# Kernel tuning notes

Measured on AMD Instinct MI355X. Metric: run time of the kernel, lower is better.

The kernel has to match this reference:

```python
import jax, jax.numpy as jnp
import numpy as np

B, S, A, C, M, CE = 2, 8, 24000, 80, 20, 7
POS_TH, NEG_TH = 0.5, 0.4
V0, V1 = 0.1, 0.2              # SSD encode variances
SL1_BETA = 1.0 / 9.0
ALPHA, GAMMA = 0.25, 2.0
CB_BETA = 0.9999
EPS = 1e-7


def point_form(cf):
    # (cx,cy,w,h) -> (x1,y1,x2,y2)
    return jnp.concatenate([cf[..., :2] - cf[..., 2:] * 0.5, cf[..., :2] + cf[..., 2:] * 0.5], -1)


def jaccard(a, b):
    # a: [M,4], b: [A,4] point form -> IoU [M,A]
    lt = jnp.maximum(a[:, None, :2], b[None, :, :2])
    rb = jnp.minimum(a[:, None, 2:], b[None, :, 2:])
    wh = jnp.clip(rb - lt, 0.0)
    inter = wh[..., 0] * wh[..., 1]
    aa = (a[:, 2] - a[:, 0]) * (a[:, 3] - a[:, 1])
    ab = (b[:, 2] - b[:, 0]) * (b[:, 3] - b[:, 1])
    return inter / (aa[:, None] + ab[None, :] - inter + 1e-10)


def encode(matched, anchors_cf):
    # matched: [A,4] point form gt, anchors_cf: [A,4] center form
    g_cxcy = ((matched[:, :2] + matched[:, 2:]) * 0.5 - anchors_cf[:, :2]) / (V0 * anchors_cf[:, 2:])
    g_wh = jnp.log(jnp.clip(matched[:, 2:] - matched[:, :2], 1e-6) / anchors_cf[:, 2:]) / V1
    return jnp.concatenate([g_cxcy, g_wh], -1)


def bce(p, y):
    p = jnp.clip(p, EPS, 1.0 - EPS)
    return -(y * jnp.log(p) + (1.0 - y) * jnp.log1p(-p))


def match_one(gtb, gtl, count, anchors_pf, anchors_cf):
    # SSD-style match with ignore band: conf in {-1 ignore, 0 background, i+1 positive matched to gt i}
    valid = jnp.arange(M) < count
    iou = jnp.where(valid[:, None], jaccard(gtb, anchors_pf), -1.0)  # [M,A]
    best_prior_idx = jnp.argmax(iou, axis=1)                         # best anchor per gt
    best_truth_iou = jnp.max(iou, axis=0)                            # best gt per anchor
    best_truth_idx = jnp.argmax(iou, axis=0)
    sidx = jnp.where(valid, best_prior_idx, A)                       # out-of-range -> dropped
    best_truth_iou = best_truth_iou.at[sidx].set(2.0, mode='drop')   # force each gt's best anchor positive
    best_truth_idx = best_truth_idx.at[sidx].set(jnp.arange(M), mode='drop')
    conf = (best_truth_idx + 1).astype(jnp.int32)                    # dummy labels = gt index
    conf = jnp.where(best_truth_iou < POS_TH, -1, conf)
    conf = jnp.where(best_truth_iou < NEG_TH, 0, conf)
    loc = encode(gtb[best_truth_idx], anchors_cf)
    has = count > 0
    conf = jnp.where(has, conf, -1)                                  # empty frame -> all ignore
    loc = jnp.where(has, loc, 0.0)
    # gather per-anchor multi-hot labels: labels_bs = [zeros; gt_labels][dumy_conf]
    lab = jnp.where((conf > 0)[:, None], gtl[jnp.clip(conf - 1, 0, M - 1)], 0.0)
    return conf, loc, lab


def setup_inputs() -> dict:
    key = jax.random.key(0)
    ks = jax.random.split(key, 10)
    confidence = jax.random.normal(ks[0], (B, S, A, C), jnp.float32)
    predicted_locations = jax.random.normal(ks[1], (B, S, A, 4), jnp.float32)
    gc = jax.random.uniform(ks[2], (B, S, M, 2))
    gw = jax.random.uniform(ks[3], (B, S, M, 2), minval=0.05, maxval=0.4)
    gt_boxes = jnp.clip(jnp.concatenate([gc - gw * 0.5, gc + gw * 0.5], -1), 0.0, 1.0)
    gt_labels = (jax.random.uniform(ks[4], (B, S, M, C)) < 0.05).astype(jnp.float32)
    counts = jax.random.randint(ks[5], (B, S), 0, M + 1, jnp.int32)
    ac = jax.random.uniform(ks[6], (A, 2))
    aw = jax.random.uniform(ks[7], (A, 2), minval=0.02, maxval=0.3)
    anchors = jnp.concatenate([ac, aw], -1)  # center form (cx,cy,w,h)
    ego_preds = jax.random.normal(ks[8], (B, S, CE), jnp.float32)
    ego_labels = jax.random.randint(ks[9], (B, S), 0, CE, jnp.int32)
    cls_num_list = jax.random.randint(jax.random.fold_in(key, 11), (C,), 1, 10000, jnp.int32)
    return {"confidence": confidence, "predicted_locations": predicted_locations,
            "gt_boxes": gt_boxes, "gt_labels": gt_labels, "counts": counts,
            "anchors": anchors, "ego_preds": ego_preds, "ego_labels": ego_labels,
            "cls_num_list": cls_num_list}


def reference(confidence, predicted_locations, gt_boxes, gt_labels, counts, anchors, ego_preds, ego_labels, cls_num_list):
    preds = jax.nn.sigmoid(confidence)
    anchors_pf = point_form(anchors)
    flat = lambda x: x.reshape((B * S,) + x.shape[2:])
    conf_t, loc_t, lab_t = jax.vmap(match_one, in_axes=(0, 0, 0, None, None))(
        flat(gt_boxes), flat(gt_labels), counts.reshape(-1), anchors_pf, anchors)
    labels_bin = jax.lax.stop_gradient(conf_t.reshape(B, S, A).astype(jnp.float32))
    gt_locations = jax.lax.stop_gradient(loc_t.reshape(B, S, A, 4))
    all_labels = jax.lax.stop_gradient(lab_t.reshape(B, S, A, C))

    pos = (labels_bin > 0).astype(jnp.float32)
    num_pos = jnp.maximum(1.0, pos.sum())
    n = jnp.abs(predicted_locations - gt_locations)
    sl1 = jnp.where(n < SL1_BETA, 0.5 * n * n / SL1_BETA, n - 0.5 * SL1_BETA)
    regression_loss = (sl1 * pos[..., None]).sum() / (num_pos * 4.0)

    # class-balanced focal loss (module hardcodes gamma=1 inside sigmoid_cb_focal_loss)
    cmask = (labels_bin > -1).astype(jnp.float32)[..., None]
    w = (1.0 - CB_BETA) / (1.0 - jnp.power(jnp.float32(CB_BETA), cls_num_list.astype(jnp.float32)))
    w = w / w.sum()
    y = all_labels
    pt = preds * y + (1.0 - preds) * (1.0 - y)
    cb = w * y + (1.0 - CB_BETA) * (1.0 - y)
    cls_loss = (bce(preds, y) * cb * (1.0 - pt) * cmask).sum() / num_pos

    # ego focal loss (replicates original get_one_hot_labels column semantics)
    ep = jax.nn.sigmoid(ego_preds)
    evalid = ego_labels > -1
    col = (jnp.where(evalid[..., None], jax.nn.one_hot(ego_labels, CE), 0.0).sum((0, 1)) > 0).astype(jnp.float32)
    oh = jnp.broadcast_to(col, ep.shape)
    af = ALPHA * oh + (1.0 - ALPHA) * (1.0 - oh)
    ept = ep * oh + (1.0 - ep) * (1.0 - oh)
    n_ego = evalid.sum().astype(jnp.float32)
    ego_sum = (bce(ep, oh) * af * (1.0 - ept) ** GAMMA * evalid[..., None].astype(jnp.float32)).sum()
    ego_loss = jnp.where(n_ego > 0, ego_sum / jnp.maximum(n_ego, 1.0), 0.0)

    return regression_loss, cls_loss / 8.0 + ego_loss / 4.0
```

## Files before the change

kernel.cpp:

```cpp
#include <hip/hip_runtime.h>
#include <math.h>

#define NB 2
#define NS 8
#define NA 24000
#define NC 80
#define NM 20
#define NCE 7
#define NBS (NB*NS)
#define CPB 75
#define APC (NA/CPB)
#define F4PC (APC*NC/4)

#define POS_TH 0.5f
#define NEG_TH 0.4f
#define OMB 1e-4f

__device__ inline unsigned long long packKey(float f, unsigned idx) {
    unsigned u = __float_as_uint(f);
    u = (u & 0x80000000u) ? ~u : (u | 0x80000000u);
    return ((unsigned long long)u << 32) | (unsigned long long)(0xFFFFFFFFu - idx);
}

__global__ void __launch_bounds__(256)
k_iou(const float* __restrict__ gtb, const int* __restrict__ counts,
      const float* __restrict__ anchors,
      float* __restrict__ bt_iou, int* __restrict__ bt_idx,
      unsigned long long* __restrict__ chunkbest,
      double* __restrict__ acc, int* __restrict__ npos) {
    int bid = blockIdx.x;
    int bs = bid / CPB;
    int chunk = bid % CPB;
    int t = threadIdx.x;
    int cnt = counts[bs];

    if (bid == 0 && t == 0) { acc[0] = 0.0; acc[1] = 0.0; *npos = 0; }

    __shared__ float sg[NM][5];
    if (t < NM) {
        const float* g = gtb + ((size_t)bs * NM + t) * 4;
        float x1 = g[0], y1 = g[1], x2 = g[2], y2 = g[3];
        sg[t][0] = x1; sg[t][1] = y1; sg[t][2] = x2; sg[t][3] = y2;
        sg[t][4] = (x2 - x1) * (y2 - y1);
    }
    __syncthreads();

    unsigned long long bp[NM];
    #pragma unroll
    for (int m = 0; m < NM; m++) bp[m] = 0ULL;

    int a0 = chunk * APC;
    for (int a = a0 + t; a < a0 + APC; a += 256) {
        float4 cf = ((const float4*)anchors)[a];
        float ax1 = cf.x - cf.z * 0.5f, ay1 = cf.y - cf.w * 0.5f;
        float ax2 = cf.x + cf.z * 0.5f, ay2 = cf.y + cf.w * 0.5f;
        float aarea = (ax2 - ax1) * (ay2 - ay1);
        float best = -1.0f; int bm = 0;
        #pragma unroll
        for (int m = 0; m < NM; m++) {
            if (m < cnt) {
                float ltx = fmaxf(sg[m][0], ax1), lty = fmaxf(sg[m][1], ay1);
                float rbx = fminf(sg[m][2], ax2), rby = fminf(sg[m][3], ay2);
                float wx = fmaxf(rbx - ltx, 0.0f), wy = fmaxf(rby - lty, 0.0f);
                float inter = wx * wy;
                float iou = inter / (sg[m][4] + aarea - inter + 1e-10f);
                if (iou > best) { best = iou; bm = m; }
                unsigned long long k = packKey(iou, (unsigned)a);
                if (k > bp[m]) bp[m] = k;
            }
        }
        bt_iou[(size_t)bs * NA + a] = best;
        bt_idx[(size_t)bs * NA + a] = bm;
    }

    __shared__ unsigned long long sk[4][NM];
    int wave = t >> 6, lane = t & 63;
    for (int m = 0; m < cnt; m++) {
        unsigned long long k = bp[m];
        #pragma unroll
        for (int off = 32; off > 0; off >>= 1) {
            unsigned long long o = __shfl_xor(k, off);
            if (o > k) k = o;
        }
        if (lane == 0) sk[wave][m] = k;
    }
    __syncthreads();
    if (t < NM) {
        unsigned long long k = 0ULL;
        if (t < cnt) {
            k = sk[0][t];
            if (sk[1][t] > k) k = sk[1][t];
            if (sk[2][t] > k) k = sk[2][t];
            if (sk[3][t] > k) k = sk[3][t];
        }
        chunkbest[bid * NM + t] = k;
    }
}

__global__ void __launch_bounds__(256)
k_match(const float* __restrict__ gtb, const int* __restrict__ counts,
        const float* __restrict__ anchors, const float* __restrict__ ploc,
        const float* __restrict__ gtl, const float* __restrict__ logits,
        const int* __restrict__ cls_num,
        const unsigned long long* __restrict__ chunkbest,
        const float* __restrict__ bt_iou, const int* __restrict__ bt_idx,
        double* __restrict__ acc, int* __restrict__ npos) {
    int bid = blockIdx.x;
    int bs = bid / CPB;
    int chunk = bid % CPB;
    int t = threadIdx.x;
    int cnt = counts[bs];

    __shared__ float sg[NM][4];
    __shared__ unsigned abest[NM];
    __shared__ float wsh[NC];
    __shared__ float wsum_sh;
    __shared__ float smask[APC];
    if (t < NM) {
        const float* g = gtb + ((size_t)bs * NM + t) * 4;
        sg[t][0] = g[0]; sg[t][1] = g[1]; sg[t][2] = g[2]; sg[t][3] = g[3];
    }
    if (t < NC) {
        float n = (float)cls_num[t];
        wsh[t] = OMB / (1.0f - powf(0.9999f, n));
    }
    if (t < NM && t < cnt) {
        unsigned long long k = 0ULL;
        for (int c = 0; c < CPB; c++) {
            unsigned long long o = chunkbest[(bs * CPB + c) * NM + t];
            if (o > k) k = o;
        }
        abest[t] = 0xFFFFFFFFu - (unsigned)(k & 0xFFFFFFFFull);
    }
    __syncthreads();
    if (t == 0) {
        float s = 0.0f;
        for (int c = 0; c < NC; c++) s += wsh[c];
        wsum_sh = s;
    }
    __syncthreads();
    if (t < NC) wsh[t] = wsh[t] / wsum_sh;

    const float SL1B = 1.0f / 9.0f;
    float regsum = 0.0f, corrsum = 0.0f;
    int pcnt = 0;
    int a0 = chunk * APC;
    for (int al = t; al < APC; al += 256) {
        int a = a0 + al;
        size_t ia = (size_t)bs * NA + a;
        float iou = bt_iou[ia];
        int idx = bt_idx[ia];
        for (int m = 0; m < cnt; m++) {
            if (abest[m] == (unsigned)a) { iou = 2.0f; idx = m; }
        }
        int code;
        if (cnt == 0) code = -1;
        else if (iou < NEG_TH) code = 0;
        else if (iou < POS_TH) code = -1;
        else code = idx + 1;
        smask[al] = (code == -1) ? 0.0f : 1.0f;
        if (code > 0) {
            pcnt++;
            float4 cf = ((const float4*)anchors)[a];
            float mx1 = sg[idx][0], my1 = sg[idx][1], mx2 = sg[idx][2], my2 = sg[idx][3];
            float g0 = ((mx1 + mx2) * 0.5f - cf.x) / (0.1f * cf.z);
            float g1 = ((my1 + my2) * 0.5f - cf.y) / (0.1f * cf.w);
            float g2 = logf(fmaxf(mx2 - mx1, 1e-6f) / cf.z) / 0.2f;
            float g3 = logf(fmaxf(my2 - my1, 1e-6f) / cf.w) / 0.2f;
            float4 p = ((const float4*)ploc)[ia];
            float n0 = fabsf(p.x - g0), n1 = fabsf(p.y - g1);
            float n2 = fabsf(p.z - g2), n3 = fabsf(p.w - g3);
            float s0 = n0 < SL1B ? 0.5f * n0 * n0 / SL1B : n0 - 0.5f * SL1B;
            float s1 = n1 < SL1B ? 0.5f * n1 * n1 / SL1B : n1 - 0.5f * SL1B;
            float s2 = n2 < SL1B ? 0.5f * n2 * n2 / SL1B : n2 - 0.5f * SL1B;
            float s3 = n3 < SL1B ? 0.5f * n3 * n3 / SL1B : n3 - 0.5f * SL1B;
            regsum += s0 + s1 + s2 + s3;

            const float4* yrow = (const float4*)(gtl + ((size_t)(bs * NM + idx)) * NC);
            const float4* xrow = (const float4*)(logits + ia * NC);
            #pragma unroll 4
            for (int c4 = 0; c4 < NC / 4; c4++) {
                float4 y4 = yrow[c4];
                if (y4.x > 0.5f || y4.y > 0.5f || y4.z > 0.5f || y4.w > 0.5f) {
                    float4 x4 = xrow[c4];
                    float yv[4] = {y4.x, y4.y, y4.z, y4.w};
                    float xv[4] = {x4.x, x4.y, x4.z, x4.w};
                    #pragma unroll
                    for (int j = 0; j < 4; j++) {
                        if (yv[j] > 0.5f) {
                            float x = xv[j];
                            float e = __expf(-x);
                            float s = 1.0f + e;
                            float pr = __builtin_amdgcn_rcpf(s);
                            float ls = __logf(s);
                            corrsum += ls * wsh[c4 * 4 + j] * (e * pr)
                                     - OMB * (x + ls) * pr;
                        }
                    }
                }
            }
        }
    }
    __syncthreads();

    const float4* x4p = (const float4*)logits + ((size_t)bs * NA + a0) * (NC / 4);
    float bgsum = 0.0f;
    #pragma unroll
    for (int g = 0; g < 5; g++) {
        float4 xs[5];
        float  ms[5];
        #pragma unroll
        for (int j = 0; j < 5; j++) {
            int i = t + (g * 5 + j) * 256;
            ms[j] = smask[i / 20];
            xs[j] = x4p[i];
        }
        #pragma unroll
        for (int j = 0; j < 5; j++) {
            float xv[4] = {xs[j].x, xs[j].y, xs[j].z, xs[j].w};
            float tsum = 0.0f;
            #pragma unroll
            for (int jj = 0; jj < 4; jj++) {
                float x = xv[jj];
                float e = __expf(-x);
                float s = 1.0f + e;
                float pr = __builtin_amdgcn_rcpf(s);
                float ls = __logf(s);
                tsum += (x + ls) * pr;
            }
            bgsum = fmaf(ms[j], tsum, bgsum);
        }
    }
    float clssum = corrsum + OMB * bgsum;

    #pragma unroll
    for (int off = 32; off > 0; off >>= 1) {
        regsum += __shfl_xor(regsum, off);
        clssum += __shfl_xor(clssum, off);
        pcnt   += __shfl_xor(pcnt, off);
    }
    __shared__ float sf[4], sc[4];
    __shared__ int   si[4];
    int wave = t >> 6, lane = t & 63;
    if (lane == 0) { sf[wave] = regsum; sc[wave] = clssum; si[wave] = pcnt; }
    __syncthreads();
    if (t == 0) {
        atomicAdd(&acc[0], (double)(sf[0] + sf[1] + sf[2] + sf[3]));
        atomicAdd(&acc[1], (double)(sc[0] + sc[1] + sc[2] + sc[3]));
        atomicAdd(npos, si[0] + si[1] + si[2] + si[3]);
    }
}

__global__ void k_final(const float* __restrict__ ego_preds, const int* __restrict__ ego_labels,
                        const double* __restrict__ acc, const int* __restrict__ npos,
                        float* __restrict__ out) {
    __shared__ float scol[NCE];
    __shared__ float sred[128];
    __shared__ int   sval[128];
    const float EPSF = 1e-7f;
    int t = threadIdx.x;
    if (t < NCE) {
        float c = 0.0f;
        for (int i = 0; i < NBS; i++) {
            int l = ego_labels[i];
            if (l > -1 && l == t) c = 1.0f;
        }
        scol[t] = c;
    }
    __syncthreads();

    float term = 0.0f;
    if (t < NBS * NCE) {
        int bs = t / NCE, e = t % NCE;
        int lbl = ego_labels[bs];
        if (lbl > -1) {
            float x = ego_preds[t];
            float ep = 1.0f / (1.0f + expf(-x));
            float oh = scol[e];
            float af = 0.25f * oh + 0.75f * (1.0f - oh);
            float ept = ep * oh + (1.0f - ep) * (1.0f - oh);
            float epc = fminf(fmaxf(ep, EPSF), 1.0f - EPSF);
            float bce = -(oh * logf(epc) + (1.0f - oh) * log1pf(-epc));
            float om = 1.0f - ept;
            term = bce * af * om * om;
        }
    }
    sred[t] = term;
    sval[t] = (t < NBS && ego_labels[t] > -1) ? 1 : 0;
    __syncthreads();
    for (int off = 64; off > 0; off >>= 1) {
        if (t < off) { sred[t] += sred[t + off]; sval[t] += sval[t + off]; }
        __syncthreads();
    }
    if (t == 0) {
        float esum = sred[0];
        int ne = sval[0];
        float ego = (ne > 0) ? esum / (float)(ne > 1 ? ne : 1) : 0.0f;
        double npd = (double)(*npos);
        if (npd < 1.0) npd = 1.0;
        out[0] = (float)(acc[0] / (npd * 4.0));
        out[1] = (float)(acc[1] / npd / 8.0 + (double)ego / 4.0);
    }
}

extern "C" void kernel_launch(void* const* d_in, const int* in_sizes, int n_in,
                              void* d_out, int out_size, void* d_ws, size_t ws_size,
                              hipStream_t stream) {
    const float* confidence = (const float*)d_in[0];
    const float* ploc       = (const float*)d_in[1];
    const float* gtb        = (const float*)d_in[2];
    const float* gtl        = (const float*)d_in[3];
    const int*   counts     = (const int*)d_in[4];
    const float* anchors    = (const float*)d_in[5];
    const float* ego_preds  = (const float*)d_in[6];
    const int*   ego_labels = (const int*)d_in[7];
    const int*   cls_num    = (const int*)d_in[8];
    float* out = (float*)d_out;

    char* ws = (char*)d_ws;
    double* acc  = (double*)ws;
    int* npos    = (int*)(ws + 16);
    unsigned long long* chunkbest = (unsigned long long*)(ws + 64);
    float* bt_iou = (float*)(ws + 64 + 192000);
    int*   bt_idx = (int*)(ws + 64 + 192000 + 1536000);

    k_iou<<<NBS * CPB, 256, 0, stream>>>(gtb, counts, anchors, bt_iou, bt_idx,
                                         chunkbest, acc, npos);
    k_match<<<NBS * CPB, 256, 0, stream>>>(gtb, counts, anchors, ploc, gtl, confidence,
                                           cls_num, chunkbest, bt_iou, bt_idx, acc, npos);
    k_final<<<1, 128, 0, stream>>>(ego_preds, ego_labels, acc, npos, out);
}
```

Baseline: 271.9 us.

## Split background class pass into its own grid and hoist per-sample prep

A single-block prep kernel now computes, once, the class-balanced weights and the per-ground-truth best-anchor reduction over chunks. Before, every match block redid both. The match kernel writes a per-anchor mask into the IoU buffer instead of shared memory. A new grid-stride kernel with 2000 blocks then streams all logits to compute the masked background focal term. The goal is to remove redundant serial reductions and to spread the bandwidth-heavy logits read over more blocks. The cost is two extra kernel launches and a global round trip for the mask.

```diff
diff --git a/kernel.cpp b/kernel.cpp
--- a/kernel.cpp
+++ b/kernel.cpp
@@ -10,11 +10,14 @@
 #define NBS (NB*NS)
 #define CPB 75
 #define APC (NA/CPB)
-#define F4PC (APC*NC/4)
 
 #define POS_TH 0.5f
 #define NEG_TH 0.4f
 #define OMB 1e-4f
+
+#define CLS_BLOCKS 2000
+#define CLS_GSZ (CLS_BLOCKS*256)
+#define CLS_PT 15
 
 __device__ inline unsigned long long packKey(float f, unsigned idx) {
     unsigned u = __float_as_uint(f);
@@ -26,15 +29,12 @@
 k_iou(const float* __restrict__ gtb, const int* __restrict__ counts,
       const float* __restrict__ anchors,
       float* __restrict__ bt_iou, int* __restrict__ bt_idx,
-      unsigned long long* __restrict__ chunkbest,
-      double* __restrict__ acc, int* __restrict__ npos) {
+      unsigned long long* __restrict__ chunkbest) {
     int bid = blockIdx.x;
     int bs = bid / CPB;
     int chunk = bid % CPB;
     int t = threadIdx.x;
     int cnt = counts[bs];
-
-    if (bid == 0 && t == 0) { acc[0] = 0.0; acc[1] = 0.0; *npos = 0; }
 
     __shared__ float sg[NM][5];
     if (t < NM) {
@@ -97,13 +97,43 @@
     }
 }
 
+__global__ void k_prep(const int* __restrict__ cls_num,
+                       const unsigned long long* __restrict__ chunkbest,
+                       float* __restrict__ wsn, unsigned* __restrict__ gbest,
+                       double* __restrict__ acc, int* __restrict__ npos) {
+    __shared__ float wsh[NC];
+    __shared__ float wsum_sh;
+    int t = threadIdx.x;
+    if (t == 0) { acc[0] = 0.0; acc[1] = 0.0; *npos = 0; }
+    if (t < NC) {
+        float n = (float)cls_num[t];
+        wsh[t] = OMB / (1.0f - powf(0.9999f, n));
+    }
+    if (t < NBS * NM) {
+        int bs = t / NM, m = t % NM;
+        unsigned long long k = 0ULL;
+        for (int c = 0; c < CPB; c++) {
+            unsigned long long o = chunkbest[(bs * CPB + c) * NM + m];
+            if (o > k) k = o;
+        }
+        gbest[t] = 0xFFFFFFFFu - (unsigned)(k & 0xFFFFFFFFull);
+    }
+    __syncthreads();
+    if (t == 0) {
+        float s = 0.0f;
+        for (int c = 0; c < NC; c++) s += wsh[c];
+        wsum_sh = s;
+    }
+    __syncthreads();
+    if (t < NC) wsn[t] = wsh[t] / wsum_sh;
+}
+
 __global__ void __launch_bounds__(256)
 k_match(const float* __restrict__ gtb, const int* __restrict__ counts,
         const float* __restrict__ anchors, const float* __restrict__ ploc,
         const float* __restrict__ gtl, const float* __restrict__ logits,
-        const int* __restrict__ cls_num,
-        const unsigned long long* __restrict__ chunkbest,
-        const float* __restrict__ bt_iou, const int* __restrict__ bt_idx,
+        const float* __restrict__ wsn, const unsigned* __restrict__ gbest,
+        float* bt_iou , const int* __restrict__ bt_idx,
         double* __restrict__ acc, int* __restrict__ npos) {
     int bid = blockIdx.x;
     int bs = bid / CPB;
@@ -113,33 +143,12 @@
 
     __shared__ float sg[NM][4];
     __shared__ unsigned abest[NM];
-    __shared__ float wsh[NC];
-    __shared__ float wsum_sh;
-    __shared__ float smask[APC];
     if (t < NM) {
         const float* g = gtb + ((size_t)bs * NM + t) * 4;
         sg[t][0] = g[0]; sg[t][1] = g[1]; sg[t][2] = g[2]; sg[t][3] = g[3];
-    }
-    if (t < NC) {
-        float n = (float)cls_num[t];
-        wsh[t] = OMB / (1.0f - powf(0.9999f, n));
-    }
-    if (t < NM && t < cnt) {
-        unsigned long long k = 0ULL;
-        for (int c = 0; c < CPB; c++) {
-            unsigned long long o = chunkbest[(bs * CPB + c) * NM + t];
-            if (o > k) k = o;
-        }
-        abest[t] = 0xFFFFFFFFu - (unsigned)(k & 0xFFFFFFFFull);
-    }
-    __syncthreads();
-    if (t == 0) {
-        float s = 0.0f;
-        for (int c = 0; c < NC; c++) s += wsh[c];
-        wsum_sh = s;
-    }
-    __syncthreads();
-    if (t < NC) wsh[t] = wsh[t] / wsum_sh;
+        abest[t] = gbest[bs * NM + t];
+    }
+    __syncthreads();
 
     const float SL1B = 1.0f / 9.0f;
     float regsum = 0.0f, corrsum = 0.0f;
@@ -158,7 +167,7 @@
         else if (iou < NEG_TH) code = 0;
         else if (iou < POS_TH) code = -1;
         else code = idx + 1;
-        smask[al] = (code == -1) ? 0.0f : 1.0f;
+        bt_iou[ia] = (code == -1) ? 0.0f : 1.0f;
         if (code > 0) {
             pcnt++;
             float4 cf = ((const float4*)anchors)[a];
@@ -193,7 +202,7 @@
                             float s = 1.0f + e;
                             float pr = __builtin_amdgcn_rcpf(s);
                             float ls = __logf(s);
-                            corrsum += ls * wsh[c4 * 4 + j] * (e * pr)
+                            corrsum += ls * wsn[c4 * 4 + j] * (e * pr)
                                      - OMB * (x + ls) * pr;
                         }
                     }
@@ -201,18 +210,39 @@
             }
         }
     }
-    __syncthreads();
-
-    const float4* x4p = (const float4*)logits + ((size_t)bs * NA + a0) * (NC / 4);
+
+    #pragma unroll
+    for (int off = 32; off > 0; off >>= 1) {
+        regsum  += __shfl_xor(regsum, off);
+        corrsum += __shfl_xor(corrsum, off);
+        pcnt    += __shfl_xor(pcnt, off);
+    }
+    __shared__ float sf[4], sc[4];
+    __shared__ int   si[4];
+    int wave = t >> 6, lane = t & 63;
+    if (lane == 0) { sf[wave] = regsum; sc[wave] = corrsum; si[wave] = pcnt; }
+    __syncthreads();
+    if (t == 0) {
+        atomicAdd(&acc[0], (double)(sf[0] + sf[1] + sf[2] + sf[3]));
+        atomicAdd(&acc[1], (double)(sc[0] + sc[1] + sc[2] + sc[3]));
+        atomicAdd(npos, si[0] + si[1] + si[2] + si[3]);
+    }
+}
+
+__global__ void __launch_bounds__(256, 8)
+k_cls(const float* __restrict__ logits, const float* __restrict__ cmask,
+      double* __restrict__ acc) {
+    int gid = blockIdx.x * 256 + threadIdx.x;
+    const float4* x4p = (const float4*)logits;
     float bgsum = 0.0f;
     #pragma unroll
-    for (int g = 0; g < 5; g++) {
+    for (int g = 0; g < 3; g++) {
         float4 xs[5];
         float  ms[5];
         #pragma unroll
         for (int j = 0; j < 5; j++) {
-            int i = t + (g * 5 + j) * 256;
-            ms[j] = smask[i / 20];
+            int i = gid + (g * 5 + j) * CLS_GSZ;
+            ms[j] = cmask[i / 20];
             xs[j] = x4p[i];
         }
         #pragma unroll
@@ -231,24 +261,14 @@
             bgsum = fmaf(ms[j], tsum, bgsum);
         }
     }
-    float clssum = corrsum + OMB * bgsum;
 
     #pragma unroll
-    for (int off = 32; off > 0; off >>= 1) {
-        regsum += __shfl_xor(regsum, off);
-        clssum += __shfl_xor(clssum, off);
-        pcnt   += __shfl_xor(pcnt, off);
-    }
-    __shared__ float sf[4], sc[4];
-    __shared__ int   si[4];
-    int wave = t >> 6, lane = t & 63;
-    if (lane == 0) { sf[wave] = regsum; sc[wave] = clssum; si[wave] = pcnt; }
-    __syncthreads();
-    if (t == 0) {
-        atomicAdd(&acc[0], (double)(sf[0] + sf[1] + sf[2] + sf[3]));
-        atomicAdd(&acc[1], (double)(sc[0] + sc[1] + sc[2] + sc[3]));
-        atomicAdd(npos, si[0] + si[1] + si[2] + si[3]);
-    }
+    for (int off = 32; off > 0; off >>= 1) bgsum += __shfl_xor(bgsum, off);
+    __shared__ float sb[4];
+    int t = threadIdx.x, wave = t >> 6, lane = t & 63;
+    if (lane == 0) sb[wave] = bgsum;
+    __syncthreads();
+    if (t == 0) atomicAdd(&acc[1], (double)(OMB * (sb[0] + sb[1] + sb[2] + sb[3])));
 }
 
 __global__ void k_final(const float* __restrict__ ego_preds, const int* __restrict__ ego_labels,
@@ -323,10 +343,13 @@
     unsigned long long* chunkbest = (unsigned long long*)(ws + 64);
     float* bt_iou = (float*)(ws + 64 + 192000);
     int*   bt_idx = (int*)(ws + 64 + 192000 + 1536000);
-
-    k_iou<<<NBS * CPB, 256, 0, stream>>>(gtb, counts, anchors, bt_iou, bt_idx,
-                                         chunkbest, acc, npos);
+    float* wsn    = (float*)(ws + 64 + 192000 + 1536000 + 1536000);
+    unsigned* gbest = (unsigned*)(ws + 64 + 192000 + 1536000 + 1536000 + 320);
+
+    k_iou<<<NBS * CPB, 256, 0, stream>>>(gtb, counts, anchors, bt_iou, bt_idx, chunkbest);
+    k_prep<<<1, 384, 0, stream>>>(cls_num, chunkbest, wsn, gbest, acc, npos);
     k_match<<<NBS * CPB, 256, 0, stream>>>(gtb, counts, anchors, ploc, gtl, confidence,
-                                           cls_num, chunkbest, bt_iou, bt_idx, acc, npos);
+                                           wsn, gbest, bt_iou, bt_idx, acc, npos);
+    k_cls<<<CLS_BLOCKS, 256, 0, stream>>>(confidence, bt_iou, acc);
     k_final<<<1, 128, 0, stream>>>(ego_preds, ego_labels, acc, npos, out);
 }
```

Result: slower. 305.6 us (+12.4%).

## Move unmasked background logit sum into IoU kernel and subtract ignored rows later

Applied to the files above, without the earlier changes.

The full-logit background sum moves into the first (IoU) kernel and is computed without the ignore mask, so it no longer depends on matching. The match kernel then subtracts the contribution of ignored anchors row by row. A new single-block prep kernel reduces the per-chunk partial sums, the best-anchor keys and the class weights once, instead of every match block redoing that work. This overlaps the large logit read with the IoU phase, at the cost of an extra launch and a double-precision reduction.

```diff
diff --git a/kernel.cpp b/kernel.cpp
--- a/kernel.cpp
+++ b/kernel.cpp
@@ -23,18 +23,16 @@
 }
 
 __global__ void __launch_bounds__(256)
-k_iou(const float* __restrict__ gtb, const int* __restrict__ counts,
-      const float* __restrict__ anchors,
-      float* __restrict__ bt_iou, int* __restrict__ bt_idx,
-      unsigned long long* __restrict__ chunkbest,
-      double* __restrict__ acc, int* __restrict__ npos) {
+k_main(const float* __restrict__ gtb, const int* __restrict__ counts,
+       const float* __restrict__ anchors, const float* __restrict__ logits,
+       float* __restrict__ bt_iou, int* __restrict__ bt_idx,
+       unsigned long long* __restrict__ chunkbest,
+       double* __restrict__ bgpart) {
     int bid = blockIdx.x;
     int bs = bid / CPB;
     int chunk = bid % CPB;
     int t = threadIdx.x;
     int cnt = counts[bs];
-
-    if (bid == 0 && t == 0) { acc[0] = 0.0; acc[1] = 0.0; *npos = 0; }
 
     __shared__ float sg[NM][5];
     if (t < NM) {
@@ -95,14 +93,85 @@
         }
         chunkbest[bid * NM + t] = k;
     }
+
+    const float4* x4p = (const float4*)logits + ((size_t)bs * NA + a0) * (NC / 4);
+    double bg = 0.0;
+    #pragma unroll
+    for (int g = 0; g < 5; g++) {
+        float4 xs[5];
+        #pragma unroll
+        for (int j = 0; j < 5; j++) xs[j] = x4p[t + (g * 5 + j) * 256];
+        #pragma unroll
+        for (int j = 0; j < 5; j++) {
+            float xv[4] = {xs[j].x, xs[j].y, xs[j].z, xs[j].w};
+            float tsum = 0.0f;
+            #pragma unroll
+            for (int jj = 0; jj < 4; jj++) {
+                float x = xv[jj];
+                float e = __expf(-x);
+                float s = 1.0f + e;
+                float pr = __builtin_amdgcn_rcpf(s);
+                float ls = __logf(s);
+                tsum += (x + ls) * pr;
+            }
+            bg += (double)tsum;
+        }
+    }
+    #pragma unroll
+    for (int off = 32; off > 0; off >>= 1) bg += __shfl_xor(bg, off);
+    __shared__ double sb[4];
+    if (lane == 0) sb[wave] = bg;
+    __syncthreads();
+    if (t == 0) bgpart[bid] = sb[0] + sb[1] + sb[2] + sb[3];
+}
+
+__global__ void k_prep(const int* __restrict__ cls_num,
+                       const unsigned long long* __restrict__ chunkbest,
+                       const double* __restrict__ bgpart,
+                       float* __restrict__ wsn, unsigned* __restrict__ gbest,
+                       double* __restrict__ acc, int* __restrict__ npos) {
+    __shared__ float wsh[NC];
+    __shared__ float wsum_sh;
+    __shared__ double sred[6];
+    int t = threadIdx.x;
+    if (t == 0) { acc[0] = 0.0; *npos = 0; }
+    if (t < NC) {
+        float n = (float)cls_num[t];
+        wsh[t] = OMB / (1.0f - powf(0.9999f, n));
+    }
+    if (t < NBS * NM) {
+        int bs = t / NM, m = t % NM;
+        unsigned long long k = 0ULL;
+        for (int c = 0; c < CPB; c++) {
+            unsigned long long o = chunkbest[(bs * CPB + c) * NM + m];
+            if (o > k) k = o;
+        }
+        gbest[t] = 0xFFFFFFFFu - (unsigned)(k & 0xFFFFFFFFull);
+    }
+    double b = 0.0;
+    for (int i = t; i < NBS * CPB; i += 384) b += bgpart[i];
+    #pragma unroll
+    for (int off = 32; off > 0; off >>= 1) b += __shfl_xor(b, off);
+    int wave = t >> 6, lane = t & 63;
+    if (lane == 0) sred[wave] = b;
+    __syncthreads();
+    if (t == 0) {
+        double s = 0.0;
+        for (int w = 0; w < 6; w++) s += sred[w];
+        acc[1] = (double)OMB * s;
+        float ws = 0.0f;
+        for (int c = 0; c < NC; c++) ws += wsh[c];
+        wsum_sh = ws;
+    }
+    __syncthreads();
+    if (t < NC) wsn[t] = wsh[t] / wsum_sh;
 }
 
 __global__ void __launch_bounds__(256)
 k_match(const float* __restrict__ gtb, const int* __restrict__ counts,
         const float* __restrict__ anchors, const float* __restrict__ ploc,
         const float* __restrict__ gtl, const float* __restrict__ logits,
-        const int* __restrict__ cls_num,
-        const unsigned long long* __restrict__ chunkbest,
+        const float* __restrict__ wsn, const unsigned* __restrict__ gbest,
         const float* __restrict__ bt_iou, const int* __restrict__ bt_idx,
         double* __restrict__ acc, int* __restrict__ npos) {
     int bid = blockIdx.x;
@@ -113,36 +182,15 @@
 
     __shared__ float sg[NM][4];
     __shared__ unsigned abest[NM];
-    __shared__ float wsh[NC];
-    __shared__ float wsum_sh;
-    __shared__ float smask[APC];
     if (t < NM) {
         const float* g = gtb + ((size_t)bs * NM + t) * 4;
         sg[t][0] = g[0]; sg[t][1] = g[1]; sg[t][2] = g[2]; sg[t][3] = g[3];
-    }
-    if (t < NC) {
-        float n = (float)cls_num[t];
-        wsh[t] = OMB / (1.0f - powf(0.9999f, n));
-    }
-    if (t < NM && t < cnt) {
-        unsigned long long k = 0ULL;
-        for (int c = 0; c < CPB; c++) {
-            unsigned long long o = chunkbest[(bs * CPB + c) * NM + t];
-            if (o > k) k = o;
-        }
-        abest[t] = 0xFFFFFFFFu - (unsigned)(k & 0xFFFFFFFFull);
-    }
-    __syncthreads();
-    if (t == 0) {
-        float s = 0.0f;
-        for (int c = 0; c < NC; c++) s += wsh[c];
-        wsum_sh = s;
-    }
-    __syncthreads();
-    if (t < NC) wsh[t] = wsh[t] / wsum_sh;
+        abest[t] = gbest[bs * NM + t];
+    }
+    __syncthreads();
 
     const float SL1B = 1.0f / 9.0f;
-    float regsum = 0.0f, corrsum = 0.0f;
+    float regsum = 0.0f, corrsum = 0.0f, negsum = 0.0f;
     int pcnt = 0;
     int a0 = chunk * APC;
     for (int al = t; al < APC; al += 256) {
@@ -158,7 +206,6 @@
         else if (iou < NEG_TH) code = 0;
         else if (iou < POS_TH) code = -1;
         else code = idx + 1;
-        smask[al] = (code == -1) ? 0.0f : 1.0f;
         if (code > 0) {
             pcnt++;
             float4 cf = ((const float4*)anchors)[a];
@@ -193,46 +240,34 @@
                             float s = 1.0f + e;
                             float pr = __builtin_amdgcn_rcpf(s);
                             float ls = __logf(s);
-                            corrsum += ls * wsh[c4 * 4 + j] * (e * pr)
+                            corrsum += ls * wsn[c4 * 4 + j] * (e * pr)
                                      - OMB * (x + ls) * pr;
                         }
                     }
                 }
             }
-        }
-    }
-    __syncthreads();
-
-    const float4* x4p = (const float4*)logits + ((size_t)bs * NA + a0) * (NC / 4);
-    float bgsum = 0.0f;
-    #pragma unroll
-    for (int g = 0; g < 5; g++) {
-        float4 xs[5];
-        float  ms[5];
-        #pragma unroll
-        for (int j = 0; j < 5; j++) {
-            int i = t + (g * 5 + j) * 256;
-            ms[j] = smask[i / 20];
-            xs[j] = x4p[i];
-        }
-        #pragma unroll
-        for (int j = 0; j < 5; j++) {
-            float xv[4] = {xs[j].x, xs[j].y, xs[j].z, xs[j].w};
-            float tsum = 0.0f;
-            #pragma unroll
-            for (int jj = 0; jj < 4; jj++) {
-                float x = xv[jj];
-                float e = __expf(-x);
-                float s = 1.0f + e;
-                float pr = __builtin_amdgcn_rcpf(s);
-                float ls = __logf(s);
-                tsum += (x + ls) * pr;
+        } else if (code == -1) {
+            const float4* xrow = (const float4*)(logits + ia * NC);
+            float rs = 0.0f;
+            #pragma unroll 5
+            for (int c4 = 0; c4 < NC / 4; c4++) {
+                float4 x4 = xrow[c4];
+                float xv[4] = {x4.x, x4.y, x4.z, x4.w};
+                #pragma unroll
+                for (int j = 0; j < 4; j++) {
+                    float x = xv[j];
+                    float e = __expf(-x);
+                    float s = 1.0f + e;
+                    float pr = __builtin_amdgcn_rcpf(s);
+                    float ls = __logf(s);
+                    rs += (x + ls) * pr;
+                }
             }
-            bgsum = fmaf(ms[j], tsum, bgsum);
-        }
-    }
-    float clssum = corrsum + OMB * bgsum;
-
+            negsum += rs;
+        }
+    }
+
+    float clssum = corrsum - OMB * negsum;
     #pragma unroll
     for (int off = 32; off > 0; off >>= 1) {
         regsum += __shfl_xor(regsum, off);
@@ -323,10 +358,14 @@
     unsigned long long* chunkbest = (unsigned long long*)(ws + 64);
     float* bt_iou = (float*)(ws + 64 + 192000);
     int*   bt_idx = (int*)(ws + 64 + 192000 + 1536000);
-
-    k_iou<<<NBS * CPB, 256, 0, stream>>>(gtb, counts, anchors, bt_iou, bt_idx,
-                                         chunkbest, acc, npos);
+    float* wsn    = (float*)(ws + 64 + 192000 + 1536000 + 1536000);
+    unsigned* gbest = (unsigned*)(ws + 64 + 192000 + 1536000 + 1536000 + 320);
+    double* bgpart  = (double*)(ws + 64 + 192000 + 1536000 + 1536000 + 320 + 1280);
+
+    k_main<<<NBS * CPB, 256, 0, stream>>>(gtb, counts, anchors, confidence,
+                                          bt_iou, bt_idx, chunkbest, bgpart);
+    k_prep<<<1, 384, 0, stream>>>(cls_num, chunkbest, bgpart, wsn, gbest, acc, npos);
     k_match<<<NBS * CPB, 256, 0, stream>>>(gtb, counts, anchors, ploc, gtl, confidence,
-                                           cls_num, chunkbest, bt_iou, bt_idx, acc, npos);
+                                           wsn, gbest, bt_iou, bt_idx, acc, npos);
     k_final<<<1, 128, 0, stream>>>(ego_preds, ego_labels, acc, npos, out);
 }
```

Result: slower. 305.3 us (+12.3%).

## Recompute IoU in match kernel, atomicMax per-gt best, defer positive class work

Applied to the files above, without the earlier changes.

The first kernel no longer writes per-anchor best IoU and index to global memory. It only computes each gt's best anchor and merges it with a global atomicMax, and the match kernel recomputes the per-anchor IoU argmax itself. Positive anchors are queued in shared memory, and their class correction terms are processed cooperatively after the background pass, which removes divergent per-thread 80-class loops. Logit loads use nontemporal hints, a memset replaces the in-kernel accumulator init, and launch bounds request 5 blocks per CU. The cost is duplicated IoU arithmetic, plus a shared-memory atomic and queue in the match kernel.

```diff
diff --git a/kernel.cpp b/kernel.cpp
--- a/kernel.cpp
+++ b/kernel.cpp
@@ -10,7 +10,6 @@
 #define NBS (NB*NS)
 #define CPB 75
 #define APC (NA/CPB)
-#define F4PC (APC*NC/4)
 
 #define POS_TH 0.5f
 #define NEG_TH 0.4f
@@ -22,19 +21,21 @@
     return ((unsigned long long)u << 32) | (unsigned long long)(0xFFFFFFFFu - idx);
 }
 
+typedef float v4f __attribute__((ext_vector_type(4)));
+__device__ inline float4 ntload4(const float4* p) {
+    v4f v = __builtin_nontemporal_load((const v4f*)p);
+    return make_float4(v.x, v.y, v.z, v.w);
+}
+
 __global__ void __launch_bounds__(256)
-k_iou(const float* __restrict__ gtb, const int* __restrict__ counts,
-      const float* __restrict__ anchors,
-      float* __restrict__ bt_iou, int* __restrict__ bt_idx,
-      unsigned long long* __restrict__ chunkbest,
-      double* __restrict__ acc, int* __restrict__ npos) {
+k_gbest(const float* __restrict__ gtb, const int* __restrict__ counts,
+        const float* __restrict__ anchors, unsigned long long* __restrict__ gbest) {
     int bid = blockIdx.x;
     int bs = bid / CPB;
     int chunk = bid % CPB;
     int t = threadIdx.x;
     int cnt = counts[bs];
-
-    if (bid == 0 && t == 0) { acc[0] = 0.0; acc[1] = 0.0; *npos = 0; }
+    if (cnt == 0) return;
 
     __shared__ float sg[NM][5];
     if (t < NM) {
@@ -45,38 +46,39 @@
     }
     __syncthreads();
 
-    unsigned long long bp[NM];
-    #pragma unroll
-    for (int m = 0; m < NM; m++) bp[m] = 0ULL;
-
     int a0 = chunk * APC;
-    for (int a = a0 + t; a < a0 + APC; a += 256) {
-        float4 cf = ((const float4*)anchors)[a];
-        float ax1 = cf.x - cf.z * 0.5f, ay1 = cf.y - cf.w * 0.5f;
-        float ax2 = cf.x + cf.z * 0.5f, ay2 = cf.y + cf.w * 0.5f;
-        float aarea = (ax2 - ax1) * (ay2 - ay1);
-        float best = -1.0f; int bm = 0;
-        #pragma unroll
-        for (int m = 0; m < NM; m++) {
-            if (m < cnt) {
-                float ltx = fmaxf(sg[m][0], ax1), lty = fmaxf(sg[m][1], ay1);
-                float rbx = fminf(sg[m][2], ax2), rby = fminf(sg[m][3], ay2);
-                float wx = fmaxf(rbx - ltx, 0.0f), wy = fmaxf(rby - lty, 0.0f);
-                float inter = wx * wy;
-                float iou = inter / (sg[m][4] + aarea - inter + 1e-10f);
-                if (iou > best) { best = iou; bm = m; }
-                unsigned long long k = packKey(iou, (unsigned)a);
-                if (k > bp[m]) bp[m] = k;
-            }
-        }
-        bt_iou[(size_t)bs * NA + a] = best;
-        bt_idx[(size_t)bs * NA + a] = bm;
+    bool has2 = t < (APC - 256);
+    float4 c1 = ((const float4*)anchors)[a0 + t];
+    float bx1 = c1.x - c1.z * 0.5f, by1 = c1.y - c1.w * 0.5f;
+    float bx2 = c1.x + c1.z * 0.5f, by2 = c1.y + c1.w * 0.5f;
+    float bar = (bx2 - bx1) * (by2 - by1);
+    float cx1 = 0, cy1 = 0, cx2 = 0, cy2 = 0, car = 0;
+    if (has2) {
+        float4 c2 = ((const float4*)anchors)[a0 + 256 + t];
+        cx1 = c2.x - c2.z * 0.5f; cy1 = c2.y - c2.w * 0.5f;
+        cx2 = c2.x + c2.z * 0.5f; cy2 = c2.y + c2.w * 0.5f;
+        car = (cx2 - cx1) * (cy2 - cy1);
     }
 
     __shared__ unsigned long long sk[4][NM];
     int wave = t >> 6, lane = t & 63;
     for (int m = 0; m < cnt; m++) {
-        unsigned long long k = bp[m];
+        float gx1 = sg[m][0], gy1 = sg[m][1], gx2 = sg[m][2], gy2 = sg[m][3], gar = sg[m][4];
+        float ltx = fmaxf(gx1, bx1), lty = fmaxf(gy1, by1);
+        float rbx = fminf(gx2, bx2), rby = fminf(gy2, by2);
+        float wx = fmaxf(rbx - ltx, 0.0f), wy = fmaxf(rby - lty, 0.0f);
+        float inter = wx * wy;
+        float iou = inter / (gar + bar - inter + 1e-10f);
+        unsigned long long k = packKey(iou, (unsigned)(a0 + t));
+        if (has2) {
+            float ltx2 = fmaxf(gx1, cx1), lty2 = fmaxf(gy1, cy1);
+            float rbx2 = fminf(gx2, cx2), rby2 = fminf(gy2, cy2);
+            float wx2 = fmaxf(rbx2 - ltx2, 0.0f), wy2 = fmaxf(rby2 - lty2, 0.0f);
+            float inter2 = wx2 * wy2;
+            float iou2 = inter2 / (gar + car - inter2 + 1e-10f);
+            unsigned long long k2 = packKey(iou2, (unsigned)(a0 + 256 + t));
+            if (k2 > k) k = k2;
+        }
         #pragma unroll
         for (int off = 32; off > 0; off >>= 1) {
             unsigned long long o = __shfl_xor(k, off);
@@ -85,25 +87,21 @@
         if (lane == 0) sk[wave][m] = k;
     }
     __syncthreads();
-    if (t < NM) {
-        unsigned long long k = 0ULL;
-        if (t < cnt) {
-            k = sk[0][t];
-            if (sk[1][t] > k) k = sk[1][t];
-            if (sk[2][t] > k) k = sk[2][t];
-            if (sk[3][t] > k) k = sk[3][t];
-        }
-        chunkbest[bid * NM + t] = k;
-    }
-}
-
-__global__ void __launch_bounds__(256)
+    if (t < cnt) {
+        unsigned long long k = sk[0][t];
+        if (sk[1][t] > k) k = sk[1][t];
+        if (sk[2][t] > k) k = sk[2][t];
+        if (sk[3][t] > k) k = sk[3][t];
+        atomicMax(&gbest[bs * NM + t], k);
+    }
+}
+
+__global__ void __launch_bounds__(256, 5)
 k_match(const float* __restrict__ gtb, const int* __restrict__ counts,
         const float* __restrict__ anchors, const float* __restrict__ ploc,
         const float* __restrict__ gtl, const float* __restrict__ logits,
         const int* __restrict__ cls_num,
-        const unsigned long long* __restrict__ chunkbest,
-        const float* __restrict__ bt_iou, const int* __restrict__ bt_idx,
+        const unsigned long long* __restrict__ gbest,
         double* __restrict__ acc, int* __restrict__ npos) {
     int bid = blockIdx.x;
     int bs = bid / CPB;
@@ -111,26 +109,25 @@
     int t = threadIdx.x;
     int cnt = counts[bs];
 
-    __shared__ float sg[NM][4];
+    __shared__ float sg[NM][5];
     __shared__ unsigned abest[NM];
     __shared__ float wsh[NC];
     __shared__ float wsum_sh;
     __shared__ float smask[APC];
+    __shared__ unsigned qpos[APC];
+    __shared__ int npq;
+    if (t == 0) npq = 0;
     if (t < NM) {
         const float* g = gtb + ((size_t)bs * NM + t) * 4;
-        sg[t][0] = g[0]; sg[t][1] = g[1]; sg[t][2] = g[2]; sg[t][3] = g[3];
+        float x1 = g[0], y1 = g[1], x2 = g[2], y2 = g[3];
+        sg[t][0] = x1; sg[t][1] = y1; sg[t][2] = x2; sg[t][3] = y2;
+        sg[t][4] = (x2 - x1) * (y2 - y1);
+        if (t < cnt)
+            abest[t] = 0xFFFFFFFFu - (unsigned)(gbest[bs * NM + t] & 0xFFFFFFFFull);
     }
     if (t < NC) {
         float n = (float)cls_num[t];
         wsh[t] = OMB / (1.0f - powf(0.9999f, n));
-    }
-    if (t < NM && t < cnt) {
-        unsigned long long k = 0ULL;
-        for (int c = 0; c < CPB; c++) {
-            unsigned long long o = chunkbest[(bs * CPB + c) * NM + t];
-            if (o > k) k = o;
-        }
-        abest[t] = 0xFFFFFFFFu - (unsigned)(k & 0xFFFFFFFFull);
     }
     __syncthreads();
     if (t == 0) {
@@ -142,27 +139,37 @@
     if (t < NC) wsh[t] = wsh[t] / wsum_sh;
 
     const float SL1B = 1.0f / 9.0f;
-    float regsum = 0.0f, corrsum = 0.0f;
+    float regsum = 0.0f;
     int pcnt = 0;
     int a0 = chunk * APC;
     for (int al = t; al < APC; al += 256) {
         int a = a0 + al;
-        size_t ia = (size_t)bs * NA + a;
-        float iou = bt_iou[ia];
-        int idx = bt_idx[ia];
+        float4 cf = ((const float4*)anchors)[a];
+        float ax1 = cf.x - cf.z * 0.5f, ay1 = cf.y - cf.w * 0.5f;
+        float ax2 = cf.x + cf.z * 0.5f, ay2 = cf.y + cf.w * 0.5f;
+        float aarea = (ax2 - ax1) * (ay2 - ay1);
+        float best = -1.0f; int bm = 0;
         for (int m = 0; m < cnt; m++) {
-            if (abest[m] == (unsigned)a) { iou = 2.0f; idx = m; }
+            float ltx = fmaxf(sg[m][0], ax1), lty = fmaxf(sg[m][1], ay1);
+            float rbx = fminf(sg[m][2], ax2), rby = fminf(sg[m][3], ay2);
+            float wx = fmaxf(rbx - ltx, 0.0f), wy = fmaxf(rby - lty, 0.0f);
+            float inter = wx * wy;
+            float iou = inter / (sg[m][4] + aarea - inter + 1e-10f);
+            if (iou > best) { best = iou; bm = m; }
+        }
+        for (int m = 0; m < cnt; m++) {
+            if (abest[m] == (unsigned)a) { best = 2.0f; bm = m; }
         }
         int code;
         if (cnt == 0) code = -1;
-        else if (iou < NEG_TH) code = 0;
-        else if (iou < POS_TH) code = -1;
-        else code = idx + 1;
+        else if (best < NEG_TH) code = 0;
+        else if (best < POS_TH) code = -1;
+        else code = bm + 1;
         smask[al] = (code == -1) ? 0.0f : 1.0f;
         if (code > 0) {
             pcnt++;
-            float4 cf = ((const float4*)anchors)[a];
-            float mx1 = sg[idx][0], my1 = sg[idx][1], mx2 = sg[idx][2], my2 = sg[idx][3];
+            size_t ia = (size_t)bs * NA + a;
+            float mx1 = sg[bm][0], my1 = sg[bm][1], mx2 = sg[bm][2], my2 = sg[bm][3];
             float g0 = ((mx1 + mx2) * 0.5f - cf.x) / (0.1f * cf.z);
             float g1 = ((my1 + my2) * 0.5f - cf.y) / (0.1f * cf.w);
             float g2 = logf(fmaxf(mx2 - mx1, 1e-6f) / cf.z) / 0.2f;
@@ -175,30 +182,8 @@
             float s2 = n2 < SL1B ? 0.5f * n2 * n2 / SL1B : n2 - 0.5f * SL1B;
             float s3 = n3 < SL1B ? 0.5f * n3 * n3 / SL1B : n3 - 0.5f * SL1B;
             regsum += s0 + s1 + s2 + s3;
-
-            const float4* yrow = (const float4*)(gtl + ((size_t)(bs * NM + idx)) * NC);
-            const float4* xrow = (const float4*)(logits + ia * NC);
-            #pragma unroll 4
-            for (int c4 = 0; c4 < NC / 4; c4++) {
-                float4 y4 = yrow[c4];
-                if (y4.x > 0.5f || y4.y > 0.5f || y4.z > 0.5f || y4.w > 0.5f) {
-                    float4 x4 = xrow[c4];
-                    float yv[4] = {y4.x, y4.y, y4.z, y4.w};
-                    float xv[4] = {x4.x, x4.y, x4.z, x4.w};
-                    #pragma unroll
-                    for (int j = 0; j < 4; j++) {
-                        if (yv[j] > 0.5f) {
-                            float x = xv[j];
-                            float e = __expf(-x);
-                            float s = 1.0f + e;
-                            float pr = __builtin_amdgcn_rcpf(s);
-                            float ls = __logf(s);
-                            corrsum += ls * wsh[c4 * 4 + j] * (e * pr)
-                                     - OMB * (x + ls) * pr;
-                        }
-                    }
-                }
-            }
+            int q = atomicAdd(&npq, 1);
+            qpos[q] = ((unsigned)bm << 16) | (unsigned)al;
         }
     }
     __syncthreads();
@@ -213,7 +198,7 @@
         for (int j = 0; j < 5; j++) {
             int i = t + (g * 5 + j) * 256;
             ms[j] = smask[i / 20];
-            xs[j] = x4p[i];
+            xs[j] = ntload4(&x4p[i]);
         }
         #pragma unroll
         for (int j = 0; j < 5; j++) {
@@ -231,6 +216,33 @@
             bgsum = fmaf(ms[j], tsum, bgsum);
         }
     }
+
+    float corrsum = 0.0f;
+    int nq = npq;
+    for (int i = t; i < nq * 20; i += 256) {
+        int qq = i / 20, c4 = i % 20;
+        unsigned e = qpos[qq];
+        int al = e & 0xFFFFu;
+        int m  = (int)(e >> 16);
+        float4 y4 = ((const float4*)(gtl + ((size_t)(bs * NM + m)) * NC))[c4];
+        if (y4.x > 0.5f || y4.y > 0.5f || y4.z > 0.5f || y4.w > 0.5f) {
+            float4 x4 = ((const float4*)(logits + ((size_t)bs * NA + a0 + al) * NC))[c4];
+            float yv[4] = {y4.x, y4.y, y4.z, y4.w};
+            float xv[4] = {x4.x, x4.y, x4.z, x4.w};
+            #pragma unroll
+            for (int j = 0; j < 4; j++) {
+                if (yv[j] > 0.5f) {
+                    float x = xv[j];
+                    float ee = __expf(-x);
+                    float s = 1.0f + ee;
+                    float pr = __builtin_amdgcn_rcpf(s);
+                    float ls = __logf(s);
+                    corrsum += ls * wsh[c4 * 4 + j] * (ee * pr)
+                             - OMB * (x + ls) * pr;
+                }
+            }
+        }
+    }
     float clssum = corrsum + OMB * bgsum;
 
     #pragma unroll
@@ -320,13 +332,11 @@
     char* ws = (char*)d_ws;
     double* acc  = (double*)ws;
     int* npos    = (int*)(ws + 16);
-    unsigned long long* chunkbest = (unsigned long long*)(ws + 64);
-    float* bt_iou = (float*)(ws + 64 + 192000);
-    int*   bt_idx = (int*)(ws + 64 + 192000 + 1536000);
-
-    k_iou<<<NBS * CPB, 256, 0, stream>>>(gtb, counts, anchors, bt_iou, bt_idx,
-                                         chunkbest, acc, npos);
+    unsigned long long* gbest = (unsigned long long*)(ws + 64);
+
+    hipMemsetAsync(ws, 0, 4096, stream);
+    k_gbest<<<NBS * CPB, 256, 0, stream>>>(gtb, counts, anchors, gbest);
     k_match<<<NBS * CPB, 256, 0, stream>>>(gtb, counts, anchors, ploc, gtl, confidence,
-                                           cls_num, chunkbest, bt_iou, bt_idx, acc, npos);
+                                           cls_num, gbest, acc, npos);
     k_final<<<1, 128, 0, stream>>>(ego_preds, ego_labels, acc, npos, out);
 }
```

Result: no change. 275.6 us (+1.3%).
